# Optimization experiments

Hardware: AMD Instinct MI355X
Metric: run time of the kernel (lower is better)

Reference implementation:

```python
import jax, jax.numpy as jnp
import numpy as np

B, S, D, H, E, K = 4, 2048, 512, 2048, 8, 2


def setup_inputs() -> dict:
    key = jax.random.key(0)
    k0, k1, k2, k3 = jax.random.split(key, 4)
    return {
        "x": jax.random.normal(k0, (B, S, D), jnp.float32),
        "router_w": jax.random.normal(k1, (E, D), jnp.float32) * 0.02,
        "router_b": jnp.zeros((E,), jnp.float32),
        "w1": jax.random.normal(k2, (E, D, H), jnp.float32) * 0.02,
        "b1": jnp.zeros((E, H), jnp.float32),
        "w2": jax.random.normal(k3, (E, H, D), jnp.float32) * 0.02,
        "b2": jnp.zeros((E, D), jnp.float32),
        "top_k": K,
    }


def reference(x, router_w, router_b, w1, b1, w2, b2, top_k):
    # x: [B, S, D]; eval mode (no router noise, no dropout)
    Bb, Ss, Dd = x.shape
    Ee = w1.shape[0]
    xf = x.reshape(-1, Dd)                                   # [T, D], T = B*S
    router_logits = xf @ router_w.T + router_b               # [T, E]
    top_v, top_i = jax.lax.top_k(router_logits, top_k)       # [T, K]
    rw = jax.nn.softmax(top_v, axis=-1)                      # [T, K]
    # combine[t, e] = sum_k rw[t, k] * (top_i[t, k] == e); zero for unrouted experts
    combine = jnp.sum(jax.nn.one_hot(top_i, Ee, dtype=xf.dtype) * rw[..., None], axis=1)  # [T, E]
    out = jnp.zeros_like(xf)
    for e in range(Ee):  # fixed small expert count; each iter is a dense GEMM pair
        h = jax.nn.gelu(xf @ w1[e] + b1[e], approximate=False)  # exact erf GELU like torch nn.GELU
        y = h @ w2[e] + b2[e]                                   # [T, D]
        out = out + combine[:, e:e + 1] * y
    return out.reshape(Bb, Ss, Dd), router_logits
```

## Files before the change

### kernel.cpp

```cpp
#include <hip/hip_runtime.h>
#include <hip/hip_bf16.h>

#define TTOK 8192
#define DDIM 512
#define HDIM 2048
#define NEXP 8
#define RBLK 256
#define RTOK (TTOK / RBLK)

typedef __bf16 bf16x8 __attribute__((ext_vector_type(8)));
typedef float f32x4 __attribute__((ext_vector_type(4)));
typedef unsigned short us8 __attribute__((ext_vector_type(8)));

__device__ __forceinline__ unsigned short f2bf(float f) {
  unsigned int u = __builtin_bit_cast(unsigned int, f);
  u += 0x7fffu + ((u >> 16) & 1u);
  return (unsigned short)(u >> 16);
}

__device__ __forceinline__ void gll16(const void* g, void* l) {
  __builtin_amdgcn_global_load_lds(
      (__attribute__((address_space(1))) void*)g,
      (__attribute__((address_space(3))) void*)l, 16, 0, 0);
}

__global__ __launch_bounds__(256) void k_router(
    const float* __restrict__ x, const float* __restrict__ rw,
    const float* __restrict__ rb, float* __restrict__ logits,
    unsigned short* __restrict__ xb,
    short* __restrict__ texp, unsigned short* __restrict__ tpos,
    float* __restrict__ tgate, int* __restrict__ blockcnt) {
  __shared__ int lcnt[NEXP];
  const int tid = threadIdx.x, wid = tid >> 6, lane = tid & 63;
  if (tid < NEXP) lcnt[tid] = 0;
  __syncthreads();
  float4 w0[NEXP], w1[NEXP];
  float rbv[NEXP];
#pragma unroll
  for (int e = 0; e < NEXP; ++e) {
    const float4* wp = (const float4*)(rw + e * DDIM);
    w0[e] = wp[lane * 2];
    w1[e] = wp[lane * 2 + 1];
    rbv[e] = rb[e];
  }
  const int tbase = blockIdx.x * RTOK;
  for (int it = 0; it < RTOK / 4; ++it) {
    const int t = tbase + it * 4 + wid;
    const float4* xr = (const float4*)(x + (size_t)t * DDIM);
    float4 v0 = xr[lane * 2], v1 = xr[lane * 2 + 1];
    us8 o;
    o[0] = f2bf(v0.x); o[1] = f2bf(v0.y); o[2] = f2bf(v0.z); o[3] = f2bf(v0.w);
    o[4] = f2bf(v1.x); o[5] = f2bf(v1.y); o[6] = f2bf(v1.z); o[7] = f2bf(v1.w);
    *(us8*)(xb + (size_t)t * DDIM + lane * 8) = o;
    float a[NEXP];
#pragma unroll
    for (int e = 0; e < NEXP; ++e)
      a[e] = v0.x * w0[e].x + v0.y * w0[e].y + v0.z * w0[e].z + v0.w * w0[e].w +
             v1.x * w1[e].x + v1.y * w1[e].y + v1.z * w1[e].z + v1.w * w1[e].w;
#pragma unroll
    for (int off = 32; off > 0; off >>= 1)
#pragma unroll
      for (int e = 0; e < NEXP; ++e) a[e] += __shfl_xor(a[e], off, 64);
    if (lane == 0) {
      float lg[NEXP];
#pragma unroll
      for (int e = 0; e < NEXP; ++e) lg[e] = a[e] + rbv[e];
      float4 s0, s1;
      s0.x = lg[0]; s0.y = lg[1]; s0.z = lg[2]; s0.w = lg[3];
      s1.x = lg[4]; s1.y = lg[5]; s1.z = lg[6]; s1.w = lg[7];
      ((float4*)(logits + t * NEXP))[0] = s0;
      ((float4*)(logits + t * NEXP))[1] = s1;
      int i0 = 0; float m0 = lg[0];
#pragma unroll
      for (int e = 1; e < NEXP; ++e) if (lg[e] > m0) { m0 = lg[e]; i0 = e; }
      int i1 = 0; float m1 = -3.4e38f;
#pragma unroll
      for (int e = 0; e < NEXP; ++e) if (e != i0 && lg[e] > m1) { m1 = lg[e]; i1 = e; }
      float e1 = expf(m1 - m0);
      float inv = 1.0f / (1.0f + e1);
      int p0 = atomicAdd(&lcnt[i0], 1);
      int p1 = atomicAdd(&lcnt[i1], 1);
      texp[t * 2] = (short)i0;     tpos[t * 2] = (unsigned short)p0;     tgate[t * 2] = inv;
      texp[t * 2 + 1] = (short)i1; tpos[t * 2 + 1] = (unsigned short)p1; tgate[t * 2 + 1] = e1 * inv;
    }
  }
  __syncthreads();
  if (tid < NEXP) blockcnt[blockIdx.x * NEXP + tid] = lcnt[tid];
}

__global__ __launch_bounds__(512) void k_offsets(const int* __restrict__ blockcnt,
                                                 int* __restrict__ blockbase,
                                                 int* __restrict__ counts,
                                                 int* __restrict__ offsets) {
  __shared__ int csh[NEXP];
  const int e = threadIdx.x >> 6, lane = threadIdx.x & 63;
  int carry = 0;
#pragma unroll
  for (int c = 0; c < RBLK; c += 64) {
    int v = blockcnt[(c + lane) * NEXP + e];
    int s = v;
#pragma unroll
    for (int o = 1; o < 64; o <<= 1) {
      int u = __shfl_up(s, o, 64);
      if (lane >= o) s += u;
    }
    blockbase[(c + lane) * NEXP + e] = carry + s - v;
    carry += __shfl(s, 63, 64);
  }
  if (lane == 0) csh[e] = carry;
  __syncthreads();
  if (threadIdx.x < NEXP) {
    int s = 0;
    for (int q = 0; q < (int)threadIdx.x; ++q) s += csh[q];
    offsets[threadIdx.x] = s;
    counts[threadIdx.x] = csh[threadIdx.x];
  }
}

__global__ void k_scatter(const short* __restrict__ texp, const unsigned short* __restrict__ tpos,
                          const float* __restrict__ tgate, const int* __restrict__ blockbase,
                          const int* __restrict__ offsets,
                          int* __restrict__ toklist, int* __restrict__ cidx,
                          float* __restrict__ cgate) {
  const int t = blockIdx.x * 256 + threadIdx.x;
  const int b = t / RTOK;
#pragma unroll
  for (int k = 0; k < 2; ++k) {
    const int e = (int)texp[t * 2 + k];
    const int pos = blockbase[b * NEXP + e] + (int)tpos[t * 2 + k];
    toklist[e * TTOK + pos] = t;
    cidx[t * 2 + k] = offsets[e] + pos;
    cgate[t * 2 + k] = tgate[t * 2 + k];
  }
}

__global__ void k_transpose2(const float* __restrict__ w1, const float* __restrict__ w2,
                             unsigned short* __restrict__ w1t, unsigned short* __restrict__ w2t) {
  __shared__ float tile[32][33];
  const int id = blockIdx.x;
  const float* in; unsigned short* out; int R, C, rem;
  if (id < 8192) {
    const int e = id >> 10; rem = id & 1023;
    R = DDIM; C = HDIM;
    in = w1 + (size_t)e * R * C; out = w1t + (size_t)e * R * C;
  } else {
    const int e = (id - 8192) >> 10; rem = (id - 8192) & 1023;
    R = HDIM; C = DDIM;
    in = w2 + (size_t)e * R * C; out = w2t + (size_t)e * R * C;
  }
  const int ctiles = C >> 5;
  const int c0 = (rem % ctiles) * 32, r0 = (rem / ctiles) * 32;
  const int tx = threadIdx.x, ty = threadIdx.y;
#pragma unroll
  for (int i = 0; i < 32; i += 8)
    tile[ty + i][tx] = in[(size_t)(r0 + ty + i) * C + (c0 + tx)];
  __syncthreads();
#pragma unroll
  for (int i = 0; i < 32; i += 8)
    out[(size_t)(c0 + ty + i) * R + (r0 + tx)] = f2bf(tile[tx][ty + i]);
}

template <int B>
__device__ __forceinline__ void mm_step(const unsigned char* smbase,
                                        const unsigned (&aoff)[2][2][4],
                                        const unsigned (&boff)[2][2][2],
                                        f32x4 (&acc)[4][2]) {
#pragma unroll
  for (int kk = 0; kk < 2; ++kk) {
    bf16x8 af[4], bv[2];
#pragma unroll
    for (int mi = 0; mi < 4; ++mi) af[mi] = *(const bf16x8*)(smbase + aoff[B][kk][mi]);
#pragma unroll
    for (int ni = 0; ni < 2; ++ni) bv[ni] = *(const bf16x8*)(smbase + boff[B][kk][ni]);
#pragma unroll
    for (int mi = 0; mi < 4; ++mi)
#pragma unroll
      for (int ni = 0; ni < 2; ++ni)
        acc[mi][ni] = __builtin_amdgcn_mfma_f32_16x16x32_bf16(af[mi], bv[ni], acc[mi][ni], 0, 0, 0);
  }
}

template <int PHASE>
__global__ __launch_bounds__(512, 4) void k_gemm(
    const unsigned short* __restrict__ A, const unsigned short* __restrict__ Bt,
    const float* __restrict__ bias, const int* __restrict__ counts,
    const int* __restrict__ offsets, const int* __restrict__ toklist,
    unsigned short* __restrict__ Out) {
  constexpr int K = (PHASE == 1) ? DDIM : HDIM;
  constexpr int NN = (PHASE == 1) ? HDIM : DDIM;
  constexpr int KB = K * 2;
  constexpr int NX = NN / 128;
  constexpr int NXSH = (PHASE == 1) ? 4 : 2;
  constexpr int NT = K / 64;

  const int id = blockIdx.x;
  const int e = id & 7;
  const int p = id >> 3;
  const int cnt = counts[e];
  const int m0 = (p >> NXSH) * 128;
  if (m0 >= cnt) return;
  const int n0 = (p & (NX - 1)) * 128;
  const int off = offsets[e];

  __shared__ alignas(16) unsigned char smem[2][32768];
  unsigned char* smbase = &smem[0][0];

  const int tid = threadIdx.x;
  const int wid = tid >> 6, lane = tid & 63;

  const char* src[4];
  unsigned dst[4];
#pragma unroll
  for (int i = 0; i < 4; ++i) {
    const int c = i * 8 + wid;
    const bool isA = c < 16;
    const int cc = isA ? c : c - 16;
    const int r = cc * 8 + (lane >> 3);
    const int cs = ((lane & 7) * 16) ^ ((r & 7) << 4);
    if (isA) {
      int mrow = m0 + r; if (mrow > cnt - 1) mrow = cnt - 1;
      if (PHASE == 1) {
        const int tok = toklist[(e << 13) + mrow];
        src[i] = (const char*)A + (size_t)tok * (DDIM * 2) + cs;
      } else {
        src[i] = (const char*)A + (size_t)(off + mrow) * KB + cs;
      }
    } else {
      src[i] = (const char*)Bt + (size_t)e * NN * KB + (size_t)(n0 + r) * KB + cs;
    }
    dst[i] = (isA ? 0u : 16384u) + cc * 1024;
  }

  const int wr = wid >> 2, wc = wid & 3;
  const int lr = lane & 15, lk = lane >> 4;

  unsigned aoff[2][2][4], boff[2][2][2];
#pragma unroll
  for (int b = 0; b < 2; ++b)
#pragma unroll
    for (int kk = 0; kk < 2; ++kk) {
#pragma unroll
      for (int mi = 0; mi < 4; ++mi) {
        const int r = wr * 64 + mi * 16 + lr;
        aoff[b][kk][mi] = b * 32768u + r * 128 + ((kk * 64 + lk * 16) ^ ((r & 7) << 4));
      }
#pragma unroll
      for (int ni = 0; ni < 2; ++ni) {
        const int r = wc * 32 + ni * 16 + lr;
        boff[b][kk][ni] = b * 32768u + 16384u + r * 128 + ((kk * 64 + lk * 16) ^ ((r & 7) << 4));
      }
    }

  f32x4 acc[4][2] = {};

#pragma unroll
  for (int i = 0; i < 4; ++i) gll16(src[i], smbase + dst[i]);
#pragma unroll
  for (int i = 0; i < 4; ++i) gll16(src[i] + 128, smbase + 32768u + dst[i]);

  for (int t = 0; t < NT; ++t) {
    if (t + 1 < NT) asm volatile("s_waitcnt vmcnt(4)" ::: "memory");
    else            asm volatile("s_waitcnt vmcnt(0)" ::: "memory");
    __builtin_amdgcn_s_barrier();
    __builtin_amdgcn_sched_barrier(0);
    if (t & 1) mm_step<1>(smbase, aoff, boff, acc);
    else       mm_step<0>(smbase, aoff, boff, acc);
    if (t + 2 < NT) {
      __builtin_amdgcn_s_barrier();
      __builtin_amdgcn_sched_barrier(0);
      const int kb = (t + 2) * 128;
      const unsigned bb = (t & 1) ? 32768u : 0u;
#pragma unroll
      for (int i = 0; i < 4; ++i) gll16(src[i] + kb, smbase + bb + dst[i]);
    }
  }

  const int lq = lane >> 4;
#pragma unroll
  for (int mi = 0; mi < 4; ++mi) {
#pragma unroll
    for (int ni = 0; ni < 2; ++ni) {
      const int n = n0 + wc * 32 + ni * 16 + lr;
      const float bv_ = bias[e * NN + n];
#pragma unroll
      for (int r2 = 0; r2 < 4; ++r2) {
        const int m = m0 + wr * 64 + mi * 16 + lq * 4 + r2;
        if (m < cnt) {
          if (PHASE == 1) {
            const float xv = acc[mi][ni][r2] + bv_;
            const float u = xv * (0.7978845608f + 0.0356774081f * xv * xv);
            const float g = xv / (1.0f + __expf(-2.0f * u));
            Out[(size_t)(off + m) * HDIM + n] = f2bf(g);
          } else {
            Out[(size_t)(off + m) * DDIM + n] = f2bf(acc[mi][ni][r2] + bv_);
          }
        }
      }
    }
  }
}

__global__ __launch_bounds__(256) void k_combine(const unsigned short* __restrict__ yp,
                                                 const int* __restrict__ cidx,
                                                 const float* __restrict__ cgate,
                                                 float* __restrict__ out) {
  const int t = blockIdx.x * 4 + (threadIdx.x >> 6);
  const int lane = threadIdx.x & 63;
  const int i0 = cidx[t * 2], i1 = cidx[t * 2 + 1];
  const float g0 = cgate[t * 2], g1 = cgate[t * 2 + 1];
  us8 a = *(const us8*)(yp + (size_t)i0 * DDIM + lane * 8);
  us8 b = *(const us8*)(yp + (size_t)i1 * DDIM + lane * 8);
  float o[8];
#pragma unroll
  for (int j = 0; j < 8; ++j) {
    const float va = __builtin_bit_cast(float, (unsigned)a[j] << 16);
    const float vb = __builtin_bit_cast(float, (unsigned)b[j] << 16);
    o[j] = g0 * va + g1 * vb;
  }
  float* op = out + (size_t)t * DDIM + lane * 8;
  *(float4*)op = *(float4*)o;
  *(float4*)(op + 4) = *(float4*)(o + 4);
}

extern "C" void kernel_launch(void* const* d_in, const int* in_sizes, int n_in,
                              void* d_out, int out_size, void* d_ws, size_t ws_size,
                              hipStream_t stream) {
  (void)in_sizes; (void)n_in; (void)out_size; (void)ws_size;
  const float* x  = (const float*)d_in[0];
  const float* rw = (const float*)d_in[1];
  const float* rb = (const float*)d_in[2];
  const float* w1 = (const float*)d_in[3];
  const float* b1 = (const float*)d_in[4];
  const float* w2 = (const float*)d_in[5];
  const float* b2 = (const float*)d_in[6];
  float* out = (float*)d_out;
  float* logits = out + (size_t)TTOK * DDIM;

  char* ws = (char*)d_ws;
  unsigned short* xb  = (unsigned short*)(ws + 0);
  unsigned short* w1t = (unsigned short*)(ws + 8388608);
  unsigned short* w2t = (unsigned short*)(ws + 25165824);
  unsigned short* h   = (unsigned short*)(ws + 41943040);
  int*   toklist = (int*)(ws + 109051904);
  int*   cidx    = (int*)(ws + 109314048);
  float* cgate   = (float*)(ws + 109379584);
  int*   counts  = (int*)(ws + 109445120);
  int*   offsets = (int*)(ws + 109445152);
  unsigned short* yp = w1t;
  char* rsc = ws + 41943040;
  short*          texp      = (short*)(rsc + 0);
  unsigned short* tpos      = (unsigned short*)(rsc + 32768);
  float*          tgate     = (float*)(rsc + 65536);
  int*            blockcnt  = (int*)(rsc + 131072);
  int*            blockbase = (int*)(rsc + 139264);

  k_router<<<RBLK, 256, 0, stream>>>(x, rw, rb, logits, xb, texp, tpos, tgate, blockcnt);
  k_transpose2<<<16384, dim3(32, 8), 0, stream>>>(w1, w2, w1t, w2t);
  k_offsets<<<1, 512, 0, stream>>>(blockcnt, blockbase, counts, offsets);
  k_scatter<<<TTOK / 256, 256, 0, stream>>>(texp, tpos, tgate, blockbase, offsets,
                                            toklist, cidx, cgate);

  k_gemm<1><<<(HDIM / 128) * (TTOK / 128) * NEXP, 512, 0, stream>>>(
      xb, w1t, b1, counts, offsets, toklist, h);
  k_gemm<2><<<(DDIM / 128) * (TTOK / 128) * NEXP, 512, 0, stream>>>(
      h, w2t, b2, counts, offsets, nullptr, yp);
  k_combine<<<TTOK / 4, 256, 0, stream>>>(yp, cidx, cgate, out);
}
```

Before: 282.2 us.

## Fuse router with weight transpose and widen first expert GEMM tile to 128x256

Merges the router kernel and the weight transpose/bf16 conversion into one launch, with the extra blocks doing the transpose, so one kernel launch goes away and the two independent jobs can overlap. Replaces the templated first-phase GEMM with a dedicated kernel using 128x256 tiles (4x4 MFMA fragments per wave), which halves the number of blocks and reuses each A tile across more output columns. The new GEMM1 is single-buffered with a sync per k-step and loses the previous double-buffered prefetch pipeline, which risks exposing load latency. The larger accumulator array also raises register pressure.

Measured after the change: 267.2 us. 5.3% less time.

```diff
diff --git a/kernel.cpp b/kernel.cpp
--- a/kernel.cpp
+++ b/kernel.cpp
@@ -24,23 +24,51 @@
       (__attribute__((address_space(3))) void*)l, 16, 0, 0);
 }
 
-__global__ __launch_bounds__(256) void k_router(
+__global__ __launch_bounds__(256) void k_routrans(
     const float* __restrict__ x, const float* __restrict__ rw,
     const float* __restrict__ rb, float* __restrict__ logits,
     unsigned short* __restrict__ xb,
     short* __restrict__ texp, unsigned short* __restrict__ tpos,
-    float* __restrict__ tgate, int* __restrict__ blockcnt) {
+    float* __restrict__ tgate, int* __restrict__ blockcnt,
+    const float* __restrict__ w1, const float* __restrict__ w2,
+    unsigned short* __restrict__ w1t, unsigned short* __restrict__ w2t) {
+  const int tid = threadIdx.x;
+  if (blockIdx.x >= RBLK) {
+    __shared__ float tile[32][33];
+    const int id = blockIdx.x - RBLK;
+    const float* in; unsigned short* out; int R, C, rem;
+    if (id < 8192) {
+      const int e = id >> 10; rem = id & 1023;
+      R = DDIM; C = HDIM;
+      in = w1 + (size_t)e * R * C; out = w1t + (size_t)e * R * C;
+    } else {
+      const int e = (id - 8192) >> 10; rem = (id - 8192) & 1023;
+      R = HDIM; C = DDIM;
+      in = w2 + (size_t)e * R * C; out = w2t + (size_t)e * R * C;
+    }
+    const int ctiles = C >> 5;
+    const int c0 = (rem % ctiles) * 32, r0 = (rem / ctiles) * 32;
+    const int tx = tid & 31, ty = tid >> 5;
+#pragma unroll
+    for (int i = 0; i < 32; i += 8)
+      tile[ty + i][tx] = in[(size_t)(r0 + ty + i) * C + (c0 + tx)];
+    __syncthreads();
+#pragma unroll
+    for (int i = 0; i < 32; i += 8)
+      out[(size_t)(c0 + ty + i) * R + (r0 + tx)] = f2bf(tile[tx][ty + i]);
+    return;
+  }
   __shared__ int lcnt[NEXP];
-  const int tid = threadIdx.x, wid = tid >> 6, lane = tid & 63;
+  const int wid = tid >> 6, lane = tid & 63;
   if (tid < NEXP) lcnt[tid] = 0;
   __syncthreads();
-  float4 w0[NEXP], w1[NEXP];
+  float4 w0r[NEXP], w1r[NEXP];
   float rbv[NEXP];
 #pragma unroll
   for (int e = 0; e < NEXP; ++e) {
     const float4* wp = (const float4*)(rw + e * DDIM);
-    w0[e] = wp[lane * 2];
-    w1[e] = wp[lane * 2 + 1];
+    w0r[e] = wp[lane * 2];
+    w1r[e] = wp[lane * 2 + 1];
     rbv[e] = rb[e];
   }
   const int tbase = blockIdx.x * RTOK;
@@ -55,8 +83,8 @@
     float a[NEXP];
 #pragma unroll
     for (int e = 0; e < NEXP; ++e)
-      a[e] = v0.x * w0[e].x + v0.y * w0[e].y + v0.z * w0[e].z + v0.w * w0[e].w +
-             v1.x * w1[e].x + v1.y * w1[e].y + v1.z * w1[e].z + v1.w * w1[e].w;
+      a[e] = v0.x * w0r[e].x + v0.y * w0r[e].y + v0.z * w0r[e].z + v0.w * w0r[e].w +
+             v1.x * w1r[e].x + v1.y * w1r[e].y + v1.z * w1r[e].z + v1.w * w1r[e].w;
 #pragma unroll
     for (int off = 32; off > 0; off >>= 1)
 #pragma unroll
@@ -134,30 +162,102 @@
   }
 }
 
-__global__ void k_transpose2(const float* __restrict__ w1, const float* __restrict__ w2,
-                             unsigned short* __restrict__ w1t, unsigned short* __restrict__ w2t) {
-  __shared__ float tile[32][33];
+__global__ __launch_bounds__(512, 4) void k_gemm1(
+    const unsigned short* __restrict__ A, const unsigned short* __restrict__ Bt,
+    const float* __restrict__ bias, const int* __restrict__ counts,
+    const int* __restrict__ offsets, const int* __restrict__ toklist,
+    unsigned short* __restrict__ Out) {
+  constexpr int K = DDIM;
+  constexpr int NN = HDIM;
+  constexpr int NX = NN / 256;
+  constexpr int NT = K / 64;
+
   const int id = blockIdx.x;
-  const float* in; unsigned short* out; int R, C, rem;
-  if (id < 8192) {
-    const int e = id >> 10; rem = id & 1023;
-    R = DDIM; C = HDIM;
-    in = w1 + (size_t)e * R * C; out = w1t + (size_t)e * R * C;
-  } else {
-    const int e = (id - 8192) >> 10; rem = (id - 8192) & 1023;
-    R = HDIM; C = DDIM;
-    in = w2 + (size_t)e * R * C; out = w2t + (size_t)e * R * C;
-  }
-  const int ctiles = C >> 5;
-  const int c0 = (rem % ctiles) * 32, r0 = (rem / ctiles) * 32;
-  const int tx = threadIdx.x, ty = threadIdx.y;
-#pragma unroll
-  for (int i = 0; i < 32; i += 8)
-    tile[ty + i][tx] = in[(size_t)(r0 + ty + i) * C + (c0 + tx)];
-  __syncthreads();
-#pragma unroll
-  for (int i = 0; i < 32; i += 8)
-    out[(size_t)(c0 + ty + i) * R + (r0 + tx)] = f2bf(tile[tx][ty + i]);
+  const int e = id & 7;
+  const int p = id >> 3;
+  const int cnt = counts[e];
+  const int m0 = (p >> 3) * 128;
+  if (m0 >= cnt) return;
+  const int n0 = (p & (NX - 1)) * 256;
+  const int off = offsets[e];
+
+  __shared__ alignas(16) unsigned char smem[49152];
+
+  const int tid = threadIdx.x;
+  const int wid = tid >> 6, lane = tid & 63;
+
+  const char* src[6];
+  unsigned dst[6];
+#pragma unroll
+  for (int i = 0; i < 6; ++i) {
+    const int c = i * 8 + wid;
+    const bool isA = c < 16;
+    const int cc = isA ? c : c - 16;
+    const int r = cc * 8 + (lane >> 3);
+    const int cs = ((lane & 7) * 16) ^ ((r & 7) << 4);
+    if (isA) {
+      int mrow = m0 + r; if (mrow > cnt - 1) mrow = cnt - 1;
+      const int tok = toklist[(e << 13) + mrow];
+      src[i] = (const char*)A + (size_t)tok * (DDIM * 2) + cs;
+    } else {
+      src[i] = (const char*)Bt + (size_t)e * NN * (K * 2) + (size_t)(n0 + r) * (K * 2) + cs;
+    }
+    dst[i] = (isA ? 0u : 16384u) + cc * 1024;
+  }
+
+  const int wr = wid >> 2, wc = wid & 3;
+  const int lr = lane & 15, lk = lane >> 4;
+
+  f32x4 acc[4][4] = {};
+
+  for (int t = 0; t < NT; ++t) {
+    const int kb = t * 128;
+#pragma unroll
+    for (int i = 0; i < 6; ++i) gll16(src[i] + kb, smem + dst[i]);
+    __syncthreads();
+#pragma unroll
+    for (int kk = 0; kk < 2; ++kk) {
+      bf16x8 af[4], bv[4];
+#pragma unroll
+      for (int mi = 0; mi < 4; ++mi) {
+        const int r = wr * 64 + mi * 16 + lr;
+        const int byteo = r * 128 + ((kk * 64 + lk * 16) ^ ((r & 7) << 4));
+        af[mi] = *(const bf16x8*)(smem + byteo);
+      }
+#pragma unroll
+      for (int ni = 0; ni < 4; ++ni) {
+        const int r = wc * 64 + ni * 16 + lr;
+        const int byteo = 16384 + r * 128 + ((kk * 64 + lk * 16) ^ ((r & 7) << 4));
+        bv[ni] = *(const bf16x8*)(smem + byteo);
+      }
+#pragma unroll
+      for (int mi = 0; mi < 4; ++mi)
+#pragma unroll
+        for (int ni = 0; ni < 4; ++ni)
+          acc[mi][ni] = __builtin_amdgcn_mfma_f32_16x16x32_bf16(af[mi], bv[ni], acc[mi][ni], 0, 0, 0);
+    }
+    if (t + 1 < NT) __syncthreads();
+  }
+
+  const int lq = lane >> 4;
+#pragma unroll
+  for (int mi = 0; mi < 4; ++mi) {
+#pragma unroll
+    for (int ni = 0; ni < 4; ++ni) {
+      const int n = n0 + wc * 64 + ni * 16 + lr;
+      const float bv_ = bias[e * NN + n];
+#pragma unroll
+      for (int r2 = 0; r2 < 4; ++r2) {
+        const int m = m0 + wr * 64 + mi * 16 + lq * 4 + r2;
+        if (m < cnt) {
+          const float xv = acc[mi][ni][r2] + bv_;
+          const float u = xv * (0.7978845608f + 0.0356774081f * xv * xv);
+          const float g = xv / (1.0f + __expf(-2.0f * u));
+          Out[(size_t)(off + m) * HDIM + n] = f2bf(g);
+        }
+      }
+    }
+  }
 }
 
 template <int B>
@@ -180,24 +280,21 @@
   }
 }
 
-template <int PHASE>
-__global__ __launch_bounds__(512, 4) void k_gemm(
+__global__ __launch_bounds__(512, 4) void k_gemm2(
     const unsigned short* __restrict__ A, const unsigned short* __restrict__ Bt,
     const float* __restrict__ bias, const int* __restrict__ counts,
-    const int* __restrict__ offsets, const int* __restrict__ toklist,
-    unsigned short* __restrict__ Out) {
-  constexpr int K = (PHASE == 1) ? DDIM : HDIM;
-  constexpr int NN = (PHASE == 1) ? HDIM : DDIM;
+    const int* __restrict__ offsets, unsigned short* __restrict__ Out) {
+  constexpr int K = HDIM;
+  constexpr int NN = DDIM;
   constexpr int KB = K * 2;
   constexpr int NX = NN / 128;
-  constexpr int NXSH = (PHASE == 1) ? 4 : 2;
   constexpr int NT = K / 64;
 
   const int id = blockIdx.x;
   const int e = id & 7;
   const int p = id >> 3;
   const int cnt = counts[e];
-  const int m0 = (p >> NXSH) * 128;
+  const int m0 = (p >> 2) * 128;
   if (m0 >= cnt) return;
   const int n0 = (p & (NX - 1)) * 128;
   const int off = offsets[e];
@@ -219,12 +316,7 @@
     const int cs = ((lane & 7) * 16) ^ ((r & 7) << 4);
     if (isA) {
       int mrow = m0 + r; if (mrow > cnt - 1) mrow = cnt - 1;
-      if (PHASE == 1) {
-        const int tok = toklist[(e << 13) + mrow];
-        src[i] = (const char*)A + (size_t)tok * (DDIM * 2) + cs;
-      } else {
-        src[i] = (const char*)A + (size_t)(off + mrow) * KB + cs;
-      }
+      src[i] = (const char*)A + (size_t)(off + mrow) * KB + cs;
     } else {
       src[i] = (const char*)Bt + (size_t)e * NN * KB + (size_t)(n0 + r) * KB + cs;
     }
@@ -285,16 +377,8 @@
 #pragma unroll
       for (int r2 = 0; r2 < 4; ++r2) {
         const int m = m0 + wr * 64 + mi * 16 + lq * 4 + r2;
-        if (m < cnt) {
-          if (PHASE == 1) {
-            const float xv = acc[mi][ni][r2] + bv_;
-            const float u = xv * (0.7978845608f + 0.0356774081f * xv * xv);
-            const float g = xv / (1.0f + __expf(-2.0f * u));
-            Out[(size_t)(off + m) * HDIM + n] = f2bf(g);
-          } else {
-            Out[(size_t)(off + m) * DDIM + n] = f2bf(acc[mi][ni][r2] + bv_);
-          }
-        }
+        if (m < cnt)
+          Out[(size_t)(off + m) * DDIM + n] = f2bf(acc[mi][ni][r2] + bv_);
       }
     }
   }
@@ -354,15 +438,15 @@
   int*            blockcnt  = (int*)(rsc + 131072);
   int*            blockbase = (int*)(rsc + 139264);
 
-  k_router<<<RBLK, 256, 0, stream>>>(x, rw, rb, logits, xb, texp, tpos, tgate, blockcnt);
-  k_transpose2<<<16384, dim3(32, 8), 0, stream>>>(w1, w2, w1t, w2t);
+  k_routrans<<<RBLK + 16384, 256, 0, stream>>>(x, rw, rb, logits, xb, texp, tpos, tgate,
+                                               blockcnt, w1, w2, w1t, w2t);
   k_offsets<<<1, 512, 0, stream>>>(blockcnt, blockbase, counts, offsets);
   k_scatter<<<TTOK / 256, 256, 0, stream>>>(texp, tpos, tgate, blockbase, offsets,
                                             toklist, cidx, cgate);
 
-  k_gemm<1><<<(HDIM / 128) * (TTOK / 128) * NEXP, 512, 0, stream>>>(
+  k_gemm1<<<(HDIM / 256) * (TTOK / 128) * NEXP, 512, 0, stream>>>(
       xb, w1t, b1, counts, offsets, toklist, h);
-  k_gemm<2><<<(DDIM / 128) * (TTOK / 128) * NEXP, 512, 0, stream>>>(
-      h, w2t, b2, counts, offsets, nullptr, yp);
+  k_gemm2<<<(DDIM / 128) * (TTOK / 128) * NEXP, 512, 0, stream>>>(
+      h, w2t, b2, counts, offsets, yp);
   k_combine<<<TTOK / 4, 256, 0, stream>>>(yp, cidx, cgate, out);
 }
```
